# Performance work log

Hardware: AMD Instinct MI355X
Metric: run time of the kernel (lower is better)

The kernel has to match this reference:

```python
import jax, jax.numpy as jnp
import numpy as np
from jax import lax

# dims
B, S, NF, E = 128, 256, 32, 4
D, H = 256, 4
DI = 2 * D            # mLSTM inner (up-projection) dim
DHM, DHS = DI // H, D // H
K = 4                 # causal conv kernel size
FF = 352              # gated FFN dim (~4/3 * D, sLSTM block post-FFN)
NE, NP = 100, 6


def _ln(x, g, b, eps=1e-5):
    mu = x.mean(-1, keepdims=True)
    v = x.var(-1, keepdims=True)
    return (x - mu) / jnp.sqrt(v + eps) * g + b


def _cconv(x, w, b):
    # depthwise causal conv1d: x [B,S,C], w [K,C], b [C]
    k = w.shape[0]
    xp = jnp.pad(x, ((0, 0), (k - 1, 0), (0, 0)))
    y = lax.conv_general_dilated(xp, w[:, None, :], (1,), 'VALID',
                                 dimension_numbers=('NWC', 'WIO', 'NWC'),
                                 feature_group_count=x.shape[-1])
    return y + b


def _headnorm(x, g, b, eps=1e-6):
    # per-head group norm: normalize over last (head-dim) axis
    mu = x.mean(-1, keepdims=True)
    v = x.var(-1, keepdims=True)
    return (x - mu) / jnp.sqrt(v + eps) * g + b


def _forward(emb_esn, emb_prof, W_in, b_in,
             m_ln_g, m_ln_b, m_Wup, m_bup, m_convW, m_convb,
             m_Wq, m_bq, m_Wk, m_bk, m_Wv, m_bv,
             m_Wi, m_bi, m_Wf, m_bf, m_skip, m_ng, m_nb, m_Wdown, m_bdown,
             s_ln_g, s_ln_b, s_convW, s_convb,
             s_Wi, s_bi, s_Wf, s_bf, s_Wz, s_bz, s_Wo, s_bo,
             s_Ri, s_Rf, s_Rz, s_Ro, s_ng, s_nb,
             f_ln_g, f_ln_b, f_Wup, f_bup, f_Wdown, f_bdown,
             h_W1, h_b1, h_W2, h_b2,
             x_sens, x_esn, x_prof):
    Bx, Sx = x_sens.shape[0], x_sens.shape[1]
    ve = jnp.broadcast_to(emb_esn[x_esn][:, None, :], (Bx, Sx, E))
    vp = jnp.broadcast_to(emb_prof[x_prof][:, None, :], (Bx, Sx, E))
    x = jnp.concatenate([x_sens, ve, vp], -1) @ W_in + b_in  # [B,S,D]

    # ---------------- block 0: mLSTM (parallel stabilized matrix memory) ----
    xn = _ln(x, m_ln_g, m_ln_b)
    up = xn @ m_Wup + m_bup
    xm, zg = jnp.split(up, 2, axis=-1)              # [B,S,DI] each
    a = jax.nn.silu(_cconv(xm, m_convW, m_convb))   # causal conv + SiLU
    q = a @ m_Wq + m_bq
    k = a @ m_Wk + m_bk
    v = xm @ m_Wv + m_bv
    gin = jnp.concatenate([q, k, v], -1)            # [B,S,3*DI]
    ipre = (gin @ m_Wi + m_bi).transpose(0, 2, 1)   # [B,H,S]
    fpre = (gin @ m_Wf + m_bf).transpose(0, 2, 1)

    def heads(t, dh):
        return t.reshape(Bx, Sx, H, dh).transpose(0, 2, 1, 3)
    qh, kh, vh = heads(q, DHM), heads(k, DHM), heads(v, DHM)  # [B,H,S,dh]

    lfg = jax.nn.log_sigmoid(fpre)
    F = jnp.cumsum(lfg, -1)                         # [B,H,S]
    logD = F[:, :, :, None] - F[:, :, None, :] + ipre[:, :, None, :]
    mask = jnp.tril(jnp.ones((Sx, Sx), bool))
    logD = jnp.where(mask, logD, -jnp.inf)
    mstab = logD.max(-1, keepdims=True)             # [B,H,S,1]
    Dm = jnp.exp(logD - mstab)
    scores = jnp.einsum('bhtd,bhsd->bhts', qh, kh) / np.sqrt(DHM).astype(np.float32)
    C = scores * Dm
    nrm = jnp.maximum(jnp.abs(C.sum(-1, keepdims=True)), jnp.exp(-mstab))
    hh = jnp.einsum('bhts,bhsd->bhtd', C, vh) / nrm
    hn = _headnorm(hh, m_ng.reshape(1, H, 1, DHM), m_nb.reshape(1, H, 1, DHM))
    hn = hn.transpose(0, 2, 1, 3).reshape(Bx, Sx, DI)
    hn = hn + m_skip * a                            # learnable skip from conv branch
    x = x + (hn * jax.nn.silu(zg)) @ m_Wdown + m_bdown

    # ---------------- block 1: sLSTM (stabilized scalar recurrent scan) -----
    xn = _ln(x, s_ln_g, s_ln_b)
    ac = jax.nn.silu(_cconv(xn, s_convW, s_convb))
    to_t = lambda t: t.reshape(Bx, Sx, H, DHS).transpose(1, 0, 2, 3)  # [S,B,H,dh]
    it = to_t(ac @ s_Wi + s_bi)
    ft = to_t(ac @ s_Wf + s_bf)
    zt = to_t(xn @ s_Wz + s_bz)
    ot = to_t(xn @ s_Wo + s_bo)

    def step(carry, xs):
        h, c, n, m = carry
        i0, f0, z0, o0 = xs
        ip = i0 + jnp.einsum('bhd,hde->bhe', h, s_Ri)
        fp = f0 + jnp.einsum('bhd,hde->bhe', h, s_Rf)
        zp = jnp.tanh(z0 + jnp.einsum('bhd,hde->bhe', h, s_Rz))
        op = jax.nn.sigmoid(o0 + jnp.einsum('bhd,hde->bhe', h, s_Ro))
        mn = jnp.maximum(fp + m, ip)
        ig = jnp.exp(ip - mn)
        fg = jnp.exp(fp + m - mn)
        c = fg * c + ig * zp
        n = fg * n + ig
        h = op * c / n
        return (h, c, n, mn), h

    init = tuple(jnp.zeros((Bx, H, DHS), x.dtype) for _ in range(4))
    _, hs = lax.scan(step, init, (it, ft, zt, ot))  # hs [S,B,H,dh]
    hs = _headnorm(hs, s_ng.reshape(1, 1, H, DHS), s_nb.reshape(1, 1, H, DHS))
    x = x + hs.transpose(1, 0, 2, 3).reshape(Bx, Sx, D)

    # gated FFN (sLSTM block post-feedforward)
    xn = _ln(x, f_ln_g, f_ln_b)
    g_, u_ = jnp.split(xn @ f_Wup + f_bup, 2, axis=-1)
    x = x + (jax.nn.gelu(g_) * u_) @ f_Wdown + f_bdown

    last = x[:, -1, :]
    return jax.nn.relu(last @ h_W1 + h_b1) @ h_W2 + h_b2


def setup_inputs() -> dict:
    key = jax.random.key(0)
    ks = iter(jax.random.split(key, 64))
    nrm = lambda sh, s=0.02: jax.random.normal(next(ks), sh, jnp.float32) * s
    z = lambda sh: jnp.zeros(sh, jnp.float32)
    o = lambda sh: jnp.ones(sh, jnp.float32)
    return dict(
        x_sens=jax.random.normal(next(ks), (B, S, NF), jnp.float32),
        x_esn=jax.random.randint(next(ks), (B,), 0, NE, jnp.int32),
        x_prof=jax.random.randint(next(ks), (B,), 0, NP, jnp.int32),
        emb_esn=nrm((NE + 1, E)), emb_prof=nrm((NP + 1, E)),
        W_in=nrm((NF + 2 * E, D)), b_in=z((D,)),
        m_ln_g=o((D,)), m_ln_b=z((D,)),
        m_Wup=nrm((D, 2 * DI)), m_bup=z((2 * DI,)),
        m_convW=nrm((K, DI)), m_convb=z((DI,)),
        m_Wq=nrm((DI, DI)), m_bq=z((DI,)),
        m_Wk=nrm((DI, DI)), m_bk=z((DI,)),
        m_Wv=nrm((DI, DI)), m_bv=z((DI,)),
        m_Wi=nrm((3 * DI, H)), m_bi=z((H,)),
        m_Wf=nrm((3 * DI, H)), m_bf=o((H,)),
        m_skip=o((DI,)), m_ng=o((DI,)), m_nb=z((DI,)),
        m_Wdown=nrm((DI, D)), m_bdown=z((D,)),
        s_ln_g=o((D,)), s_ln_b=z((D,)),
        s_convW=nrm((K, D)), s_convb=z((D,)),
        s_Wi=nrm((D, D)), s_bi=z((D,)),
        s_Wf=nrm((D, D)), s_bf=o((D,)),
        s_Wz=nrm((D, D)), s_bz=z((D,)),
        s_Wo=nrm((D, D)), s_bo=z((D,)),
        s_Ri=nrm((H, DHS, DHS)), s_Rf=nrm((H, DHS, DHS)),
        s_Rz=nrm((H, DHS, DHS)), s_Ro=nrm((H, DHS, DHS)),
        s_ng=o((D,)), s_nb=z((D,)),
        f_ln_g=o((D,)), f_ln_b=z((D,)),
        f_Wup=nrm((D, 2 * FF)), f_bup=z((2 * FF,)),
        f_Wdown=nrm((FF, D)), f_bdown=z((D,)),
        h_W1=nrm((D, 64), 0.05), h_b1=z((64,)),
        h_W2=nrm((64, 3), 0.05), h_b2=z((3,)),
    )


def reference(emb_esn, emb_prof, W_in, b_in,
              m_ln_g, m_ln_b, m_Wup, m_bup, m_convW, m_convb,
              m_Wq, m_bq, m_Wk, m_bk, m_Wv, m_bv,
              m_Wi, m_bi, m_Wf, m_bf, m_skip, m_ng, m_nb, m_Wdown, m_bdown,
              s_ln_g, s_ln_b, s_convW, s_convb,
              s_Wi, s_bi, s_Wf, s_bf, s_Wz, s_bz, s_Wo, s_bo,
              s_Ri, s_Rf, s_Rz, s_Ro, s_ng, s_nb,
              f_ln_g, f_ln_b, f_Wup, f_bup, f_Wdown, f_bdown,
              h_W1, h_b1, h_W2, h_b2,
              x_sens, x_esn, x_prof):
    return _forward(emb_esn, emb_prof, W_in, b_in,
                    m_ln_g, m_ln_b, m_Wup, m_bup, m_convW, m_convb,
                    m_Wq, m_bq, m_Wk, m_bk, m_Wv, m_bv,
                    m_Wi, m_bi, m_Wf, m_bf, m_skip, m_ng, m_nb, m_Wdown, m_bdown,
                    s_ln_g, s_ln_b, s_convW, s_convb,
                    s_Wi, s_bi, s_Wf, s_bf, s_Wz, s_bz, s_Wo, s_bo,
                    s_Ri, s_Rf, s_Rz, s_Ro, s_ng, s_nb,
                    f_ln_g, f_ln_b, f_Wup, f_bup, f_Wdown, f_bdown,
                    h_W1, h_b1, h_W2, h_b2,
                    x_sens, x_esn, x_prof)
```

## Files before the change

### kernel.cpp

```cpp
#include <hip/hip_runtime.h>
#include <cstdint>
#include <cstddef>


using u16 = unsigned short;
using u32 = unsigned int;

typedef __attribute__((ext_vector_type(8))) short short8;
typedef __attribute__((ext_vector_type(8))) unsigned short ushort8v;
typedef __attribute__((ext_vector_type(4))) float float4v;

#define DEVINL __device__ __forceinline__

DEVINL float b2f(u16 u){ u32 x = ((u32)u) << 16; return __builtin_bit_cast(float, x); }
DEVINL u16 f2b(float f){
  u32 x = __builtin_bit_cast(u32, f);
  u32 r = x + 0x7FFFu + ((x >> 16) & 1u);
  return (u16)(r >> 16);
}
DEVINL float ldval(float x){ return x; }
DEVINL float ldval(u16 x){ return b2f(x); }
DEVINL void stval(float* p, float v){ *p = v; }
DEVINL void stval(u16* p, float v){ *p = f2b(v); }

constexpr int IN_N = 56;
constexpr long long IN_SIZES[IN_N] = {
  1048576, 128, 128, 404, 28, 10240, 256, 256, 256,
  262144, 1024, 2048, 512,
  262144, 512, 262144, 512, 262144, 512,
  6144, 4, 6144, 4,
  512, 512, 512, 131072, 256,
  256, 256, 1024, 256,
  65536, 256, 65536, 256, 65536, 256, 65536, 256,
  16384, 16384, 16384, 16384,
  256, 256,
  256, 256, 180224, 704, 90112, 256,
  16384, 64, 192, 3 };

constexpr bool is_wt_input(int i){
  return i==9 || i==13 || i==15 || i==17 || i==26 || i==32 || i==34 || i==36
      || i==38 || i==48 || i==50;
}

struct CvOff { long long off[IN_N+1]; };
constexpr CvOff make_off(){
  CvOff o{};
  long long a = 0;
  for (int i = 0; i < IN_N; i++){
    o.off[i] = a;
    long long s = IN_SIZES[i];
    if (i == 1 || i == 2 || is_wt_input(i)) s = 0;
    a += s;
  }
  o.off[IN_N] = a;
  return o;
}
constexpr CvOff CVOFF = make_off();
constexpr long long CV_TOTAL = CVOFF.off[IN_N];

constexpr int WT_NW = 11;
constexpr int WTB_IN[WT_NW] = {9, 13, 15, 17, 26, 32, 34, 36, 38, 48, 50};
constexpr int WTB_K[WT_NW]  = {256,512,512,512,512,256,256,256,256,256,352};
constexpr int WTB_N[WT_NW]  = {1024,512,512,512,256,256,256,256,256,704,256};
constexpr long long WTO[WT_NW+1] = {0, 262144, 524288, 786432, 1048576, 1179648,
  1245184, 1310720, 1376256, 1441792, 1622016, 1712128};
constexpr long long WT_ELEMS = WTO[WT_NW];

constexpr long long alignup(long long x){ return ((x + 255) / 256) * 256; }
constexpr long long TOK = 32768;
constexpr long long OFF_FLAG = alignup(CV_TOTAL);
constexpr long long OFF_IP  = OFF_FLAG + 64;
constexpr long long OFF_FP  = OFF_IP  + 131072;
constexpr long long OFF_F   = OFF_FP  + 131072;
constexpr long long OFF_G   = OFF_F   + 131072;
constexpr long long OFF_M   = OFF_G   + 131072;
constexpr long long OFF_X   = OFF_M   + 131072;
constexpr long long OFF_XN  = OFF_X   + TOK*256;
constexpr long long OFF_UP  = OFF_XN  + TOK*128;
constexpr long long OFF_A   = OFF_UP  + TOK*512;
constexpr long long OFF_Q   = OFF_A   + TOK*256;
constexpr long long OFF_K   = OFF_Q   + TOK*256;
constexpr long long OFF_V   = OFF_K   + TOK*256;
constexpr long long OFF_WT  = OFF_V   + TOK*256;
constexpr long long WS_END  = OFF_WT  + WT_ELEMS/2 + 256;


__global__ void detect_kernel(const void* mlng, int* flag){
  if (threadIdx.x == 0){
    u32 u = *(const u32*)mlng;
    *flag = (u == 0x3F803F80u) ? 1 : 0;
  }
}

struct InPtrs { const void* p[IN_N]; };

__global__ __launch_bounds__(256) void convert_kernel(InPtrs ptrs, float* __restrict__ cv,
                                                      const int* __restrict__ flag){
  long long gid = (long long)blockIdx.x * 256 + threadIdx.x;
  if (gid >= CV_TOTAL) return;
  int seg = 0;
#pragma unroll
  for (int i = 1; i < IN_N; i++) seg += (gid >= CVOFF.off[i]) ? 1 : 0;
  long long local = gid - CVOFF.off[seg];
  float v;
  if (*flag) v = b2f(((const u16*)ptrs.p[seg])[local]);
  else       v = ((const float*)ptrs.p[seg])[local];
  cv[gid] = v;
}

__global__ __launch_bounds__(256) void wtrans_kernel(InPtrs ptrs, u16* __restrict__ WTb,
                                                     const int* __restrict__ flag){
  int wz = blockIdx.z;
  int K = WTB_K[wz], N = WTB_N[wz];
  int n0 = blockIdx.x * 32, k0 = blockIdx.y * 32;
  if (n0 >= N || k0 >= K) return;
  const void* W = ptrs.p[WTB_IN[wz]];
  u16* WT = WTb + WTO[wz];
  __shared__ u16 tile[32][34];
  int tx = threadIdx.x & 31, ty = threadIdx.x >> 5;
  bool bf = (*flag != 0);
#pragma unroll
  for (int i = 0; i < 4; i++){
    size_t src = (size_t)(k0 + ty + i*8)*N + n0 + tx;
    tile[ty + i*8][tx] = bf ? ((const u16*)W)[src] : f2b(((const float*)W)[src]);
  }
  __syncthreads();
#pragma unroll
  for (int i = 0; i < 4; i++)
    WT[(size_t)(n0 + ty + i*8)*K + k0 + tx] = tile[tx][ty + i*8];
}

__global__ __launch_bounds__(256) void cat_kernel(const float* __restrict__ xs,
    const int* __restrict__ xe, const int* __restrict__ xp,
    const float* __restrict__ ee, const float* __restrict__ ep,
    float* __restrict__ CAT){
  int gid = blockIdx.x * 256 + threadIdx.x;
  int c = gid % 40; int t = gid / 40; int b = t >> 8;
  float v;
  if (c < 32)      v = xs[(size_t)t*32 + c];
  else if (c < 36) v = ee[xe[b]*4 + (c - 32)];
  else             v = ep[xp[b]*4 + (c - 36)];
  CAT[(size_t)t*40 + c] = v;
}

template<typename TA, typename TC>
__global__ __launch_bounds__(256) void gemm_kernel(
    const TA* __restrict__ A, int lda,
    const float* __restrict__ Wm, const float* __restrict__ bias,
    TC* __restrict__ Cc, int ldc, const float* __restrict__ resid,
    int M, int N, int K)
{
  __shared__ float As[16][68];
  __shared__ float Bs[16][68];
  const int bm = blockIdx.y * 64, bn = blockIdx.x * 64;
  const int tid = threadIdx.x, tx = tid & 15, ty = tid >> 4;
  float acc[4][4] = {};
  for (int k0 = 0; k0 < K; k0 += 16){
#pragma unroll
    for (int i = 0; i < 4; i++){
      int idx = tid + i*256;
      int m = idx >> 4, kq = idx & 15;
      As[kq][m] = (k0 + kq < K) ? ldval(A[(size_t)(bm + m)*lda + k0 + kq]) : 0.f;
      int kk = idx >> 6, n = idx & 63;
      Bs[kk][n] = (k0 + kk < K) ? Wm[(size_t)(k0 + kk)*N + bn + n] : 0.f;
    }
    __syncthreads();
#pragma unroll
    for (int kq = 0; kq < 16; kq++){
      float av[4], bv[4];
#pragma unroll
      for (int i = 0; i < 4; i++) av[i] = As[kq][ty*4 + i];
#pragma unroll
      for (int j = 0; j < 4; j++) bv[j] = Bs[kq][tx*4 + j];
#pragma unroll
      for (int i = 0; i < 4; i++)
#pragma unroll
        for (int j = 0; j < 4; j++) acc[i][j] += av[i]*bv[j];
    }
    __syncthreads();
  }
#pragma unroll
  for (int i = 0; i < 4; i++){
    int m = bm + ty*4 + i;
#pragma unroll
    for (int j = 0; j < 4; j++){
      int n = bn + tx*4 + j;
      float v = acc[i][j] + bias[n];
      if (resid) v += resid[(size_t)m*ldc + n];
      stval(&Cc[(size_t)m*ldc + n], v);
    }
  }
}

template<typename TC>
__global__ __launch_bounds__(256) void gemm_mfma(
    const u16* __restrict__ A, int lda,
    const u16* __restrict__ WT,
    const float* __restrict__ bias,
    TC* __restrict__ Cc, int ldc, const float* __restrict__ resid,
    int N, int K)
{
  __shared__ alignas(16) u16 As[128*40];
  __shared__ alignas(16) u16 Bs[128*40];
  const int bm = blockIdx.y * 128, bn = blockIdx.x * 128;
  const int tid = threadIdx.x;
  const int w = tid >> 6, lane = tid & 63, lm = lane & 15, q = lane >> 4;
  const int wm = w >> 1, wn = w & 1;
  float4v acc[4][4] = {};
  for (int k0 = 0; k0 < K; k0 += 32){
    __syncthreads();
#pragma unroll
    for (int c = tid; c < 512; c += 256){
      int r = c >> 2, ch = c & 3;
      *(uint4*)&As[r*40 + ch*8] = *(const uint4*)&A[(size_t)(bm + r)*lda + k0 + ch*8];
      int n = bn + r;
      uint4 bv = {0u,0u,0u,0u};
      if (n < N) bv = *(const uint4*)&WT[(size_t)n*K + k0 + ch*8];
      *(uint4*)&Bs[r*40 + ch*8] = bv;
    }
    __syncthreads();
    short8 a[4], b[4];
#pragma unroll
    for (int i = 0; i < 4; i++)
      a[i] = *(const short8*)&As[(wm*64 + i*16 + lm)*40 + q*8];
#pragma unroll
    for (int j = 0; j < 4; j++)
      b[j] = *(const short8*)&Bs[(wn*64 + j*16 + lm)*40 + q*8];
#pragma unroll
    for (int i = 0; i < 4; i++)
#pragma unroll
      for (int j = 0; j < 4; j++)
        acc[i][j] = __builtin_amdgcn_mfma_f32_16x16x32_bf16(a[i], b[j], acc[i][j], 0, 0, 0);
  }
#pragma unroll
  for (int i = 0; i < 4; i++){
#pragma unroll
    for (int j = 0; j < 4; j++){
      int col = bn + wn*64 + j*16 + lm;
      if (col < N){
#pragma unroll
        for (int r = 0; r < 4; r++){
          int row = bm + wm*64 + i*16 + q*4 + r;
          float v = acc[i][j][r] + bias[col];
          if (resid) v += resid[(size_t)row*ldc + col];
          stval(&Cc[(size_t)row*ldc + col], v);
        }
      }
    }
  }
}

__global__ __launch_bounds__(256) void ln_kernel(const float* __restrict__ Xin,
    const float* __restrict__ g, const float* __restrict__ b,
    u16* __restrict__ out, float eps){
  int t = blockIdx.x*4 + (threadIdx.x >> 6);
  int e = threadIdx.x & 63;
  float4 v = *(const float4*)&Xin[(size_t)t*256 + e*4];
  float su = v.x + v.y + v.z + v.w;
#pragma unroll
  for (int o = 32; o > 0; o >>= 1) su += __shfl_xor(su, o, 64);
  float mu = su * (1.f/256.f);
  float d0 = v.x - mu, d1 = v.y - mu, d2 = v.z - mu, d3 = v.w - mu;
  float sq = d0*d0 + d1*d1 + d2*d2 + d3*d3;
#pragma unroll
  for (int o = 32; o > 0; o >>= 1) sq += __shfl_xor(sq, o, 64);
  float rstd = rsqrtf(sq * (1.f/256.f) + eps);
  float4 gv = *(const float4*)&g[e*4];
  float4 bv = *(const float4*)&b[e*4];
  ushort4 o4;
  o4.x = f2b(d0*rstd*gv.x + bv.x);
  o4.y = f2b(d1*rstd*gv.y + bv.y);
  o4.z = f2b(d2*rstd*gv.z + bv.z);
  o4.w = f2b(d3*rstd*gv.w + bv.w);
  *(ushort4*)&out[(size_t)t*256 + e*4] = o4;
}

__global__ __launch_bounds__(256) void conv_silu_kernel(const u16* __restrict__ Xc, int ldx, int C,
    const float* __restrict__ w, const float* __restrict__ bias, u16* __restrict__ Y){
  int nc = C >> 3;
  long long gid = (long long)blockIdx.x * 256 + threadIdx.x;
  int c8 = (int)(gid % nc) * 8; long long t = gid / nc;
  int s = (int)(t & 255);
  float acc[8];
#pragma unroll
  for (int i = 0; i < 8; i++) acc[i] = bias[c8 + i];
#pragma unroll
  for (int j = 0; j < 4; j++){
    int so = s - 3 + j;
    if (so >= 0){
      ushort8v xv = *(const ushort8v*)&Xc[(size_t)(t - 3 + j)*ldx + c8];
#pragma unroll
      for (int i = 0; i < 8; i++) acc[i] += b2f(xv[i]) * w[j*C + c8 + i];
    }
  }
  ushort8v o8;
#pragma unroll
  for (int i = 0; i < 8; i++) o8[i] = f2b(acc[i] / (1.f + __expf(-acc[i])));
  *(ushort8v*)&Y[(size_t)t*C + c8] = o8;
}

__global__ __launch_bounds__(256) void gates_kernel(
    const u16* __restrict__ Q, const u16* __restrict__ Kb, const u16* __restrict__ V,
    const float* __restrict__ Wi, const float* __restrict__ bi,
    const float* __restrict__ Wf, const float* __restrict__ bf,
    float* __restrict__ IP, float* __restrict__ FP){
  int t = blockIdx.x; int tid = threadIdx.x;
  int o = tid & 7, seg = tid >> 3;
  int b = t >> 8, s = t & 255;
  int g = o & 3;
  const float* Wg = (o >= 4) ? Wf : Wi;
  float part = 0.f;
#pragma unroll
  for (int i = 0; i < 6; i++){
    int k8 = seg*48 + i*8;
    const u16* src; int off;
    if (k8 < 512){ src = Q; off = k8; }
    else if (k8 < 1024){ src = Kb; off = k8 - 512; }
    else { src = V; off = k8 - 1024; }
    ushort8v gv = *(const ushort8v*)&src[(size_t)t*512 + off];
#pragma unroll
    for (int j = 0; j < 8; j++) part += b2f(gv[j]) * Wg[(k8 + j)*4 + g];
  }
  __shared__ float red[256];
  red[tid] = part; __syncthreads();
  if (tid < 8){
    float tot = 0.f;
    for (int ss = 0; ss < 32; ss++) tot += red[ss*8 + tid];
    int gg = tid & 3;
    if (tid < 4) IP[(b*4 + gg)*256 + s] = tot + bi[gg];
    else         FP[(b*4 + gg)*256 + s] = tot + bf[gg];
  }
}

__global__ __launch_bounds__(256) void fscan_kernel(const float* __restrict__ IP,
    const float* __restrict__ FP, float* __restrict__ Fo, float* __restrict__ Go,
    float* __restrict__ Mo){
  int bh = blockIdx.x; int s = threadIdx.x;
  int idx = bh*256 + s;
  __shared__ float buf[256];
  float fp = FP[idx];
  float lfg = fminf(fp, 0.f) - log1pf(expf(-fabsf(fp)));
  float v = lfg;
  buf[s] = v; __syncthreads();
  for (int off = 1; off < 256; off <<= 1){
    float tv = (s >= off) ? buf[s - off] : 0.f;
    __syncthreads();
    v += tv; buf[s] = v;
    __syncthreads();
  }
  float Fv = v;
  float g = IP[idx] - Fv;
  float mv = g;
  buf[s] = mv; __syncthreads();
  for (int off = 1; off < 256; off <<= 1){
    float tv = (s >= off) ? buf[s - off] : -3.0e38f;
    __syncthreads();
    mv = fmaxf(mv, tv); buf[s] = mv;
    __syncthreads();
  }
  Fo[idx] = Fv; Go[idx] = g; Mo[idx] = mv;
}

__global__ __launch_bounds__(256) void attn_kernel(
    const u16* __restrict__ Q, const u16* __restrict__ Kb, const u16* __restrict__ V,
    const float* __restrict__ G, const float* __restrict__ Mx, const float* __restrict__ F,
    const u16* __restrict__ Ab, const u16* __restrict__ UPb,
    const float* __restrict__ ng, const float* __restrict__ nb,
    const float* __restrict__ skip, u16* __restrict__ Yb)
{
  int bh = blockIdx.y, b = bh >> 2, h = bh & 3;
  int tt = blockIdx.x, t0 = tt * 64;
  int tid = threadIdx.x;
  int w = tid >> 6, lane = tid & 63, lm = lane & 15, q = lane >> 4;
  int gbase = bh * 256;

  __shared__ alignas(16) u16 Qs[64*136];
  __shared__ alignas(16) u16 Ks[64*136];
  __shared__ alignas(16) u16 Vt[128*72];
  __shared__ alignas(16) u16 Ps[64*72];
  __shared__ float rs[64];

#pragma unroll
  for (int c = tid; c < 1024; c += 256){
    int r = c >> 4, ch = c & 15;
    *(uint4*)&Qs[r*136 + ch*8] =
      *(const uint4*)&Q[((size_t)(b*256 + t0 + r))*512 + h*128 + ch*8];
  }
  if (tid < 64) rs[tid] = 0.f;

  float mrow[4];
#pragma unroll
  for (int r = 0; r < 4; r++) mrow[r] = Mx[gbase + t0 + w*16 + q*4 + r];

  float4v acc2[8] = {};
  const float scale = 0.08838834764831845f;

  for (int ss = 0; ss <= tt; ss++){
    int s0 = ss * 64;
    __syncthreads();
#pragma unroll
    for (int c = tid; c < 1024; c += 256){
      int r = c >> 4, ch = c & 15;
      *(uint4*)&Ks[r*136 + ch*8] =
        *(const uint4*)&Kb[((size_t)(b*256 + s0 + r))*512 + h*128 + ch*8];
    }
#pragma unroll
    for (int c = tid; c < 1024; c += 256){
      int sl = c & 63, db = c >> 6;
      ushort8v v = *(const ushort8v*)&V[((size_t)(b*256 + s0 + sl))*512 + h*128 + db*8];
#pragma unroll
      for (int j = 0; j < 8; j++) Vt[(db*8 + j)*72 + sl] = v[j];
    }
    __syncthreads();
    float4v sacc[4] = {};
#pragma unroll
    for (int k0 = 0; k0 < 128; k0 += 32){
      short8 a = *(const short8*)&Qs[(w*16 + lm)*136 + k0 + q*8];
#pragma unroll
      for (int j = 0; j < 4; j++){
        short8 bb = *(const short8*)&Ks[(j*16 + lm)*136 + k0 + q*8];
        sacc[j] = __builtin_amdgcn_mfma_f32_16x16x32_bf16(a, bb, sacc[j], 0, 0, 0);
      }
    }
    float rp[4] = {0.f, 0.f, 0.f, 0.f};
#pragma unroll
    for (int j = 0; j < 4; j++){
      int scol = s0 + j*16 + lm;
      float gq = G[gbase + scol];
#pragma unroll
      for (int r = 0; r < 4; r++){
        int trow = t0 + w*16 + q*4 + r;
        float cval = (scol <= trow) ? sacc[j][r]*scale*__expf(gq - mrow[r]) : 0.f;
        Ps[(w*16 + q*4 + r)*72 + j*16 + lm] = f2b(cval);
        rp[r] += cval;
      }
    }
#pragma unroll
    for (int r = 0; r < 4; r++){
#pragma unroll
      for (int m = 1; m < 16; m <<= 1) rp[r] += __shfl_xor(rp[r], m, 16);
      if (lm == 0) rs[w*16 + q*4 + r] += rp[r];
    }
#pragma unroll
    for (int k0 = 0; k0 < 64; k0 += 32){
      short8 a = *(const short8*)&Ps[(w*16 + lm)*72 + k0 + q*8];
#pragma unroll
      for (int jd = 0; jd < 8; jd++){
        short8 bb = *(const short8*)&Vt[(jd*16 + lm)*72 + k0 + q*8];
        acc2[jd] = __builtin_amdgcn_mfma_f32_16x16x32_bf16(a, bb, acc2[jd], 0, 0, 0);
      }
    }
  }
  __syncthreads();
#pragma unroll
  for (int r = 0; r < 4; r++){
    int rl = w*16 + q*4 + r;
    int t = t0 + rl;
    float Fv = F[gbase + t];
    float nrm = fmaxf(fabsf(rs[rl]), __expf(-(Fv + mrow[r])));
    float inv = 1.f / nrm;
    float vv[8];
    float su = 0.f;
#pragma unroll
    for (int jd = 0; jd < 8; jd++){ vv[jd] = acc2[jd][r]*inv; su += vv[jd]; }
#pragma unroll
    for (int m = 1; m < 16; m <<= 1) su += __shfl_xor(su, m, 16);
    float mu = su * (1.f/128.f);
    float sq = 0.f;
#pragma unroll
    for (int jd = 0; jd < 8; jd++){ vv[jd] -= mu; sq += vv[jd]*vv[jd]; }
#pragma unroll
    for (int m = 1; m < 16; m <<= 1) sq += __shfl_xor(sq, m, 16);
    float rstd = rsqrtf(sq * (1.f/128.f) + 1e-6f);
#pragma unroll
    for (int jd = 0; jd < 8; jd++){
      int c = h*128 + jd*16 + lm;
      float hv = vv[jd]*rstd*ng[c] + nb[c];
      float av = b2f(Ab[(size_t)t*512 + c]);
      float zg = b2f(UPb[(size_t)t*1024 + 512 + c]);
      float sz = zg / (1.f + __expf(-zg));
      Yb[(size_t)t*512 + c] = f2b((hv + skip[c]*av)*sz);
    }
  }
}

__global__ __launch_bounds__(64) void scan_kernel(
    const float* __restrict__ IT, const float* __restrict__ FT,
    const float* __restrict__ ZT, const float* __restrict__ OT,
    const float* __restrict__ Ri, const float* __restrict__ Rf,
    const float* __restrict__ Rz, const float* __restrict__ Ro,
    const float* __restrict__ sng, const float* __restrict__ snb,
    float* __restrict__ Xr){
  int bh = blockIdx.x; int b = bh >> 2, h = bh & 3;
  int e = threadIdx.x;
  float r0[64], r1[64], r2[64], r3[64];
  const float* Rp0 = Ri + h*4096; const float* Rp1 = Rf + h*4096;
  const float* Rp2 = Rz + h*4096; const float* Rp3 = Ro + h*4096;
#pragma unroll
  for (int d = 0; d < 64; d++){
    r0[d] = Rp0[d*64 + e];
    r1[d] = Rp1[d*64 + e];
    r2[d] = Rp2[d*64 + e];
    r3[d] = Rp3[d*64 + e];
  }
  float gw = sng[h*64 + e], bw = snb[h*64 + e];
  float hS = 0.f, cS = 0.f, nS = 0.f, mS = 0.f;
  size_t rowbase = ((size_t)b*256)*256 + h*64 + e;
  float i0 = IT[rowbase], f0 = FT[rowbase], z0 = ZT[rowbase], o0 = OT[rowbase];
  float xc = Xr[rowbase];
  for (int s = 0; s < 256; s++){
    float iN = 0.f, fN = 0.f, zN = 0.f, oN = 0.f, xN = 0.f;
    if (s < 255){
      size_t nrow = rowbase + (size_t)(s + 1)*256;
      iN = IT[nrow]; fN = FT[nrow]; zN = ZT[nrow]; oN = OT[nrow]; xN = Xr[nrow];
    }
    float ai0 = 0.f, ai1 = 0.f, af0 = 0.f, af1 = 0.f;
    float az0 = 0.f, az1 = 0.f, ao0 = 0.f, ao1 = 0.f;
#pragma unroll
    for (int d = 0; d < 64; d += 2){
      float h0 = __builtin_bit_cast(float,
          __builtin_amdgcn_readlane(__builtin_bit_cast(int, hS), d));
      float h1 = __builtin_bit_cast(float,
          __builtin_amdgcn_readlane(__builtin_bit_cast(int, hS), d + 1));
      ai0 += h0*r0[d]; ai1 += h1*r0[d+1];
      af0 += h0*r1[d]; af1 += h1*r1[d+1];
      az0 += h0*r2[d]; az1 += h1*r2[d+1];
      ao0 += h0*r3[d]; ao1 += h1*r3[d+1];
    }
    float ip = i0 + ai0 + ai1;
    float fp = f0 + af0 + af1;
    float zp = tanhf(z0 + az0 + az1);
    float op = 1.f / (1.f + __expf(-(o0 + ao0 + ao1)));
    float mn = fmaxf(fp + mS, ip);
    float ig = __expf(ip - mn);
    float fg = __expf(fp + mS - mn);
    cS = fg*cS + ig*zp;
    nS = fg*nS + ig;
    mS = mn;
    hS = op * cS / nS;
    float su = hS, sq = hS*hS;
#pragma unroll
    for (int o = 32; o > 0; o >>= 1){
      su += __shfl_xor(su, o, 64);
      sq += __shfl_xor(sq, o, 64);
    }
    float mu = su * (1.f/64.f);
    float var = fmaxf(sq * (1.f/64.f) - mu*mu, 0.f);
    float nv = (hS - mu) * rsqrtf(var + 1e-6f) * gw + bw;
    Xr[rowbase + (size_t)s*256] = xc + nv;
    xc = xN; i0 = iN; f0 = fN; z0 = zN; o0 = oN;
  }
}

__global__ __launch_bounds__(256) void ffn_act_kernel(const u16* __restrict__ GU,
                                                      u16* __restrict__ P){
  long long gid = (long long)blockIdx.x * 256 + threadIdx.x;
  int j8 = (int)(gid % 44) * 8; long long t = gid / 44;
  ushort8v gv = *(const ushort8v*)&GU[(size_t)t*704 + j8];
  ushort8v uv = *(const ushort8v*)&GU[(size_t)t*704 + 352 + j8];
  ushort8v o8;
#pragma unroll
  for (int i = 0; i < 8; i++){
    float g = b2f(gv[i]);
    float u = b2f(uv[i]);
    float inner = 0.7978845608028654f * (g + 0.044715f*g*g*g);
    float gel = 0.5f * g * (1.f + tanhf(inner));
    o8[i] = f2b(gel * u);
  }
  *(ushort8v*)&P[(size_t)t*352 + j8] = o8;
}

__global__ __launch_bounds__(64) void head_kernel(const float* __restrict__ X,
    const float* __restrict__ W1, const float* __restrict__ b1,
    const float* __restrict__ W2, const float* __restrict__ b2,
    void* out, const int* __restrict__ flag){
  int b = blockIdx.x, j = threadIdx.x;
  __shared__ float L[256];
  __shared__ float H1[64];
  for (int i = j; i < 256; i += 64) L[i] = X[((size_t)(b*256 + 255))*256 + i];
  __syncthreads();
  float acc = b1[j];
  for (int d = 0; d < 256; d++) acc += L[d] * W1[d*64 + j];
  H1[j] = fmaxf(acc, 0.f);
  __syncthreads();
  if (j < 3){
    float o = b2[j];
    for (int k2 = 0; k2 < 64; k2++) o += H1[k2] * W2[k2*3 + j];
    if (*flag) ((u16*)out)[b*3 + j] = f2b(o);
    else       ((float*)out)[b*3 + j] = o;
  }
}

extern "C" void kernel_launch(void* const* d_in, const int* in_sizes, int n_in,
                              void* d_out, int out_size, void* d_ws, size_t ws_size,
                              hipStream_t stream)
{
  if (n_in != IN_N) return;
  for (int i = 0; i < IN_N; i++) if ((long long)in_sizes[i] != IN_SIZES[i]) return;
  if (ws_size < (size_t)WS_END * 4) return;
  if (out_size != 384) return;

  float* ws = (float*)d_ws;
  float* cv = ws;
  auto cvp = [&](int i){ return cv + CVOFF.off[i]; };

  int*   flag = (int*)(ws + OFF_FLAG);
  float* IP   = ws + OFF_IP;
  float* FP   = ws + OFF_FP;
  float* Fb   = ws + OFF_F;
  float* Gb   = ws + OFF_G;
  float* Mb   = ws + OFF_M;
  float* X    = ws + OFF_X;
  u16*   XNb  = (u16*)(ws + OFF_XN);
  u16*   UPb  = (u16*)(ws + OFF_UP);
  u16*   Ab   = (u16*)(ws + OFF_A);
  u16*   Qb   = (u16*)(ws + OFF_Q);
  u16*   Kbb  = (u16*)(ws + OFF_K);
  u16*   Vb   = (u16*)(ws + OFF_V);
  u16*   WTb  = (u16*)(ws + OFF_WT);
  float* CAT = ws + OFF_V;
  u16*   Yb  = Qb;
  u16*   ACb = Ab;
  float* ITf = ws + OFF_K;
  float* FTf = ws + OFF_V;
  float* ZTf = ws + OFF_Q;
  float* OTf = ws + OFF_UP;
  u16*   GUb = UPb;
  u16*   Pb  = Ab;

  auto wt = [&](int widx){ return WTb + WTO[widx]; };

  InPtrs ptrs;
  for (int i = 0; i < IN_N; i++) ptrs.p[i] = d_in[i];

  const int M = 32768;
  detect_kernel<<<1, 64, 0, stream>>>(d_in[7], flag);
  int cvblocks = (int)((CV_TOTAL + 255) / 256);
  convert_kernel<<<cvblocks, 256, 0, stream>>>(ptrs, cv, flag);
  wtrans_kernel<<<dim3(32, 16, 11), 256, 0, stream>>>(ptrs, WTb, flag);
  cat_kernel<<<5120, 256, 0, stream>>>(cvp(0), (const int*)d_in[1], (const int*)d_in[2],
                                       cvp(3), cvp(4), CAT);
  gemm_kernel<float, float><<<dim3(4, 512), 256, 0, stream>>>(CAT, 40, cvp(5), cvp(6),
      X, 256, nullptr, M, 256, 40);
  ln_kernel<<<8192, 256, 0, stream>>>(X, cvp(7), cvp(8), XNb, 1e-5f);
  gemm_mfma<u16><<<dim3(8, 256), 256, 0, stream>>>(XNb, 256, wt(0), cvp(10),
      UPb, 1024, nullptr, 1024, 256);
  conv_silu_kernel<<<8192, 256, 0, stream>>>(UPb, 1024, 512, cvp(11), cvp(12), Ab);
  gemm_mfma<u16><<<dim3(4, 256), 256, 0, stream>>>(Ab, 512, wt(1), cvp(14),
      Qb, 512, nullptr, 512, 512);
  gemm_mfma<u16><<<dim3(4, 256), 256, 0, stream>>>(Ab, 512, wt(2), cvp(16),
      Kbb, 512, nullptr, 512, 512);
  gemm_mfma<u16><<<dim3(4, 256), 256, 0, stream>>>(UPb, 1024, wt(3), cvp(18),
      Vb, 512, nullptr, 512, 512);
  gates_kernel<<<M, 256, 0, stream>>>(Qb, Kbb, Vb, cvp(19), cvp(20), cvp(21), cvp(22), IP, FP);
  fscan_kernel<<<512, 256, 0, stream>>>(IP, FP, Fb, Gb, Mb);
  attn_kernel<<<dim3(4, 512), 256, 0, stream>>>(Qb, Kbb, Vb, Gb, Mb, Fb,
      Ab, UPb, cvp(24), cvp(25), cvp(23), Yb);
  gemm_mfma<float><<<dim3(2, 256), 256, 0, stream>>>(Yb, 512, wt(4), cvp(27),
      X, 256, X, 256, 512);
  ln_kernel<<<8192, 256, 0, stream>>>(X, cvp(28), cvp(29), XNb, 1e-5f);
  conv_silu_kernel<<<4096, 256, 0, stream>>>(XNb, 256, 256, cvp(30), cvp(31), ACb);
  gemm_mfma<float><<<dim3(2, 256), 256, 0, stream>>>(ACb, 256, wt(5), cvp(33),
      ITf, 256, nullptr, 256, 256);
  gemm_mfma<float><<<dim3(2, 256), 256, 0, stream>>>(ACb, 256, wt(6), cvp(35),
      FTf, 256, nullptr, 256, 256);
  gemm_mfma<float><<<dim3(2, 256), 256, 0, stream>>>(XNb, 256, wt(7), cvp(37),
      ZTf, 256, nullptr, 256, 256);
  gemm_mfma<float><<<dim3(2, 256), 256, 0, stream>>>(XNb, 256, wt(8), cvp(39),
      OTf, 256, nullptr, 256, 256);
  scan_kernel<<<512, 64, 0, stream>>>(ITf, FTf, ZTf, OTf, cvp(40), cvp(41), cvp(42), cvp(43),
      cvp(44), cvp(45), X);
  ln_kernel<<<8192, 256, 0, stream>>>(X, cvp(46), cvp(47), XNb, 1e-5f);
  gemm_mfma<u16><<<dim3(6, 256), 256, 0, stream>>>(XNb, 256, wt(9), cvp(49),
      GUb, 704, nullptr, 704, 256);
  ffn_act_kernel<<<5632, 256, 0, stream>>>(GUb, Pb);
  gemm_mfma<float><<<dim3(2, 256), 256, 0, stream>>>(Pb, 352, wt(10), cvp(51),
      X, 256, X, 256, 352);
  head_kernel<<<128, 64, 0, stream>>>(X, cvp(52), cvp(53), cvp(54), cvp(55), d_out, flag);
}
```

Measured before the change: 1.236 ms.

## Split sLSTM recurrence across four waves with LDS reduction and separate norm wave

```diff
diff --git a/kernel.cpp b/kernel.cpp
--- a/kernel.cpp
+++ b/kernel.cpp
@@ -484,7 +484,7 @@
   }
 }
 
-__global__ __launch_bounds__(64) void scan_kernel(
+__global__ __launch_bounds__(320) void scan_kernel(
     const float* __restrict__ IT, const float* __restrict__ FT,
     const float* __restrict__ ZT, const float* __restrict__ OT,
     const float* __restrict__ Ri, const float* __restrict__ Rf,
@@ -492,53 +492,99 @@
     const float* __restrict__ sng, const float* __restrict__ snb,
     float* __restrict__ Xr){
   int bh = blockIdx.x; int b = bh >> 2, h = bh & 3;
-  int e = threadIdx.x;
-  float r0[64], r1[64], r2[64], r3[64];
-  const float* Rp0 = Ri + h*4096; const float* Rp1 = Rf + h*4096;
-  const float* Rp2 = Rz + h*4096; const float* Rp3 = Ro + h*4096;
-#pragma unroll
-  for (int d = 0; d < 64; d++){
-    r0[d] = Rp0[d*64 + e];
-    r1[d] = Rp1[d*64 + e];
-    r2[d] = Rp2[d*64 + e];
-    r3[d] = Rp3[d*64 + e];
-  }
-  float gw = sng[h*64 + e], bw = snb[h*64 + e];
-  float hS = 0.f, cS = 0.f, nS = 0.f, mS = 0.f;
+  int e = threadIdx.x & 63;
+  int w = threadIdx.x >> 6;
+  __shared__ float4 part[2][4][64];
+  __shared__ float hbuf[2][64];
   size_t rowbase = ((size_t)b*256)*256 + h*64 + e;
-  float i0 = IT[rowbase], f0 = FT[rowbase], z0 = ZT[rowbase], o0 = OT[rowbase];
-  float xc = Xr[rowbase];
-  for (int s = 0; s < 256; s++){
-    float iN = 0.f, fN = 0.f, zN = 0.f, oN = 0.f, xN = 0.f;
-    if (s < 255){
-      size_t nrow = rowbase + (size_t)(s + 1)*256;
-      iN = IT[nrow]; fN = FT[nrow]; zN = ZT[nrow]; oN = OT[nrow]; xN = Xr[nrow];
-    }
-    float ai0 = 0.f, ai1 = 0.f, af0 = 0.f, af1 = 0.f;
-    float az0 = 0.f, az1 = 0.f, ao0 = 0.f, ao1 = 0.f;
-#pragma unroll
-    for (int d = 0; d < 64; d += 2){
-      float h0 = __builtin_bit_cast(float,
-          __builtin_amdgcn_readlane(__builtin_bit_cast(int, hS), d));
-      float h1 = __builtin_bit_cast(float,
-          __builtin_amdgcn_readlane(__builtin_bit_cast(int, hS), d + 1));
-      ai0 += h0*r0[d]; ai1 += h1*r0[d+1];
-      af0 += h0*r1[d]; af1 += h1*r1[d+1];
-      az0 += h0*r2[d]; az1 += h1*r2[d+1];
-      ao0 += h0*r3[d]; ao1 += h1*r3[d+1];
-    }
-    float ip = i0 + ai0 + ai1;
-    float fp = f0 + af0 + af1;
-    float zp = tanhf(z0 + az0 + az1);
-    float op = 1.f / (1.f + __expf(-(o0 + ao0 + ao1)));
-    float mn = fmaxf(fp + mS, ip);
-    float ig = __expf(ip - mn);
-    float fg = __expf(fp + mS - mn);
-    cS = fg*cS + ig*zp;
-    nS = fg*nS + ig;
-    mS = mn;
-    hS = op * cS / nS;
-    float su = hS, sq = hS*hS;
+
+  if (w < 4){
+    float r0[16], r1[16], r2[16], r3[16];
+    const float* Rp0 = Ri + h*4096 + w*1024;
+    const float* Rp1 = Rf + h*4096 + w*1024;
+    const float* Rp2 = Rz + h*4096 + w*1024;
+    const float* Rp3 = Ro + h*4096 + w*1024;
+#pragma unroll
+    for (int d = 0; d < 16; d++){
+      r0[d] = Rp0[d*64 + e];
+      r1[d] = Rp1[d*64 + e];
+      r2[d] = Rp2[d*64 + e];
+      r3[d] = Rp3[d*64 + e];
+    }
+    float hS = 0.f, cS = 0.f, nS = 0.f, mS = 0.f;
+    float i0 = 0.f, f0 = 0.f, z0 = 0.f, o0 = 0.f;
+    if (w == 0){ i0 = IT[rowbase]; f0 = FT[rowbase]; z0 = ZT[rowbase]; o0 = OT[rowbase]; }
+    for (int s = 0; s < 256; s++){
+      float iN = 0.f, fN = 0.f, zN = 0.f, oN = 0.f;
+      if (w == 0 && s < 255){
+        size_t nr = rowbase + (size_t)(s + 1)*256;
+        iN = IT[nr]; fN = FT[nr]; zN = ZT[nr]; oN = OT[nr];
+      }
+      float ai0 = 0.f, ai1 = 0.f, af0 = 0.f, af1 = 0.f;
+      float az0 = 0.f, az1 = 0.f, ao0 = 0.f, ao1 = 0.f;
+#pragma unroll
+      for (int k = 0; k < 16; k += 2){
+        float h0 = __builtin_bit_cast(float,
+            __builtin_amdgcn_readlane(__builtin_bit_cast(int, hS), w*16 + k));
+        float h1 = __builtin_bit_cast(float,
+            __builtin_amdgcn_readlane(__builtin_bit_cast(int, hS), w*16 + k + 1));
+        ai0 += h0*r0[k]; ai1 += h1*r0[k+1];
+        af0 += h0*r1[k]; af1 += h1*r1[k+1];
+        az0 += h0*r2[k]; az1 += h1*r2[k+1];
+        ao0 += h0*r3[k]; ao1 += h1*r3[k+1];
+      }
+      float4 p;
+      p.x = ai0 + ai1; p.y = af0 + af1; p.z = az0 + az1; p.w = ao0 + ao1;
+      if (w == 0){
+        p.x += i0; p.y += f0; p.z += z0; p.w += o0;
+        i0 = iN; f0 = fN; z0 = zN; o0 = oN;
+      }
+      part[s & 1][w][e] = p;
+      __syncthreads();
+      float4 q0 = part[s & 1][0][e];
+      float4 q1 = part[s & 1][1][e];
+      float4 q2 = part[s & 1][2][e];
+      float4 q3 = part[s & 1][3][e];
+      float ip = q0.x + q1.x + q2.x + q3.x;
+      float fp = q0.y + q1.y + q2.y + q3.y;
+      float zr = q0.z + q1.z + q2.z + q3.z;
+      float og = q0.w + q1.w + q2.w + q3.w;
+      float zp = 1.f - 2.f*__builtin_amdgcn_rcpf(__expf(2.f*zr) + 1.f);
+      float op = __builtin_amdgcn_rcpf(1.f + __expf(-og));
+      float mn = fmaxf(fp + mS, ip);
+      float ig = __expf(ip - mn);
+      float fg = __expf(fp + mS - mn);
+      cS = fg*cS + ig*zp;
+      nS = fg*nS + ig;
+      mS = mn;
+      hS = op * cS * __builtin_amdgcn_rcpf(nS);
+      if (w == 1) hbuf[s & 1][e] = hS;
+    }
+    __syncthreads();
+  } else {
+    float gw = sng[h*64 + e], bw = snb[h*64 + e];
+    float xp = 0.f, xc = 0.f;
+    for (int s = 0; s < 256; s++){
+      xc = Xr[rowbase + (size_t)s*256];
+      __syncthreads();
+      if (s > 0){
+        float hv = hbuf[(s - 1) & 1][e];
+        float su = hv, sq = hv*hv;
+#pragma unroll
+        for (int o = 32; o > 0; o >>= 1){
+          su += __shfl_xor(su, o, 64);
+          sq += __shfl_xor(sq, o, 64);
+        }
+        float mu = su * (1.f/64.f);
+        float var = fmaxf(sq * (1.f/64.f) - mu*mu, 0.f);
+        float nv = (hv - mu) * rsqrtf(var + 1e-6f) * gw + bw;
+        Xr[rowbase + (size_t)(s - 1)*256] = xp + nv;
+      }
+      xp = xc;
+    }
+    __syncthreads();
+    float hv = hbuf[1][e];
+    float su = hv, sq = hv*hv;
 #pragma unroll
     for (int o = 32; o > 0; o >>= 1){
       su += __shfl_xor(su, o, 64);
@@ -546,9 +592,8 @@
     }
     float mu = su * (1.f/64.f);
     float var = fmaxf(sq * (1.f/64.f) - mu*mu, 0.f);
-    float nv = (hS - mu) * rsqrtf(var + 1e-6f) * gw + bw;
-    Xr[rowbase + (size_t)s*256] = xc + nv;
-    xc = xN; i0 = iN; f0 = fN; z0 = zN; o0 = oN;
+    float nv = (hv - mu) * rsqrtf(var + 1e-6f) * gw + bw;
+    Xr[rowbase + (size_t)255*256] = xp + nv;
   }
 }
 
@@ -668,7 +713,7 @@
       ZTf, 256, nullptr, 256, 256);
   gemm_mfma<float><<<dim3(2, 256), 256, 0, stream>>>(XNb, 256, wt(8), cvp(39),
       OTf, 256, nullptr, 256, 256);
-  scan_kernel<<<512, 64, 0, stream>>>(ITf, FTf, ZTf, OTf, cvp(40), cvp(41), cvp(42), cvp(43),
+  scan_kernel<<<512, 320, 0, stream>>>(ITf, FTf, ZTf, OTf, cvp(40), cvp(41), cvp(42), cvp(43),
       cvp(44), cvp(45), X);
   ln_kernel<<<8192, 256, 0, stream>>>(X, cvp(46), cvp(47), XNb, 1e-5f);
   gemm_mfma<u16><<<dim3(6, 256), 256, 0, stream>>>(XNb, 256, wt(9), cvp(49),
```

After: 1.137 ms. 1.09x faster.
